# Optimization experiments

Hardware: AMD Instinct MI355X
Metric: run time of the kernel (lower is better)

The kernel has to match this reference:

```python
import jax, jax.numpy as jnp
import numpy as np

D_MODEL = 1024
NUM_HEADS = 16
DEPTH = D_MODEL // NUM_HEADS


def setup_inputs() -> dict:
    key = jax.random.key(0)
    ks = jax.random.split(key, 12)
    B, S = 4, 2048
    scale = 1.0 / np.sqrt(D_MODEL)
    inp = {
        "query": jax.random.normal(ks[0], (B, S, D_MODEL), jnp.float32),
        "key": jax.random.normal(ks[1], (B, S, D_MODEL), jnp.float32),
        "value": jax.random.normal(ks[2], (B, S, D_MODEL), jnp.float32),
        "mask": jnp.zeros((B, 1, 1, S), jnp.float32),  # 1.0 => masked position
        "wq": jax.random.normal(ks[3], (D_MODEL, D_MODEL), jnp.float32) * scale,
        "bq": jnp.zeros((D_MODEL,), jnp.float32),
        "wk": jax.random.normal(ks[4], (D_MODEL, D_MODEL), jnp.float32) * scale,
        "bk": jnp.zeros((D_MODEL,), jnp.float32),
        "wv": jax.random.normal(ks[5], (D_MODEL, D_MODEL), jnp.float32) * scale,
        "bv": jnp.zeros((D_MODEL,), jnp.float32),
        "wo": jax.random.normal(ks[6], (D_MODEL, D_MODEL), jnp.float32) * scale,
        "bo": jnp.zeros((D_MODEL,), jnp.float32),
    }
    return inp


def _split_heads(x, B):
    # (B, S, d_model) -> (B, H, S, depth)
    return x.reshape(B, -1, NUM_HEADS, DEPTH).transpose(0, 2, 1, 3)


def reference(query, key, value, mask, wq, bq, wk, bk, wv, bv, wo, bo):
    B, Sq, _ = query.shape
    q = _split_heads(query @ wq + bq, B)   # (B,H,Sq,dh)
    k = _split_heads(key @ wk + bk, B)     # (B,H,Sk,dh)
    v = _split_heads(value @ wv + bv, B)   # (B,H,Sk,dh)

    logits = jnp.einsum("bhqd,bhkd->bhqk", q, k) / jnp.sqrt(
        jnp.asarray(DEPTH, q.dtype))
    logits = logits + mask * (-1e9)
    attn = jax.nn.softmax(logits, axis=-1)
    ctx = jnp.einsum("bhqk,bhkd->bhqd", attn, v)
    ctx = ctx.transpose(0, 2, 1, 3).reshape(B, Sq, D_MODEL)
    return ctx @ wo + bo
```

## Files before the change

kernel.cpp:

```cpp
#include <hip/hip_runtime.h>
#include <stdint.h>


typedef unsigned short u16;
typedef __attribute__((ext_vector_type(8))) short bf16x8;
typedef __attribute__((ext_vector_type(4))) short bf16x4;
typedef __attribute__((ext_vector_type(4))) float f32x4;

#define LOG2E 1.4426950408889634f

__device__ __forceinline__ u16 f2bf(float f) {
  uint32_t u = __builtin_bit_cast(uint32_t, f);
  u += 0x7fffu + ((u >> 16) & 1u);
  return (u16)(u >> 16);
}
__device__ __forceinline__ uint32_t cvt_pk(float a, float b) {
  uint32_t r;
  asm("v_cvt_pk_bf16_f32 %0, %1, %2" : "=v"(r) : "v"(a), "v"(b));
  return r;
}
__device__ __forceinline__ void gload16(const u16* g, u16* l) {
  __builtin_amdgcn_global_load_lds(
      (const __attribute__((address_space(1))) uint32_t*)(const void*)g,
      (__attribute__((address_space(3))) uint32_t*)(void*)l, 16, 0, 0);
}
__device__ __forceinline__ f32x4 mfma16(bf16x4 a, bf16x4 b, f32x4 c) {
#if __has_builtin(__builtin_amdgcn_mfma_f32_16x16x16bf16_1k)
  return __builtin_amdgcn_mfma_f32_16x16x16bf16_1k(a, b, c, 0, 0, 0);
#else
  f32x4 d = c;
  asm volatile("v_mfma_f32_16x16x16_bf16 %0, %1, %2, %0"
               : "+v"(d) : "v"(a), "v"(b));
  return d;
#endif
}

__global__ __launch_bounds__(256) void convert_x(
    const float* __restrict__ X, u16* __restrict__ Xb)
{
  const size_t i = ((size_t)blockIdx.x * 256 + threadIdx.x) * 8;
  const float4 a = *(const float4*)(X + i);
  const float4 b = *(const float4*)(X + i + 4);
  uint4 o;
  o.x = cvt_pk(a.x, a.y); o.y = cvt_pk(a.z, a.w);
  o.z = cvt_pk(b.x, b.y); o.w = cvt_pk(b.z, b.w);
  *(uint4*)(Xb + i) = o;
}

__global__ __launch_bounds__(256) void prep_mask(
    const float* __restrict__ mask, float* __restrict__ M2)
{
  const int i = blockIdx.x * 256 + threadIdx.x;
  M2[i] = mask[i] * (-1.0e9f * LOG2E);
}

__global__ __launch_bounds__(256) void transpose_w(
    const float* __restrict__ W0, const float* __restrict__ W1,
    const float* __restrict__ W2, const float* __restrict__ W3,
    u16* __restrict__ Wt)
{
  const int z = blockIdx.z;
  const float* W = (z == 0) ? W0 : (z == 1) ? W1 : (z == 2) ? W2 : W3;
  u16* T = Wt + ((size_t)z << 20);
  const int n0 = blockIdx.x * 64, k0 = blockIdx.y * 64;
  const int tid = threadIdx.x;
  const int r = tid >> 4, c4 = (tid & 15) * 4;
  __shared__ float t[64][65];
#pragma unroll
  for (int j = 0; j < 4; ++j) {
    const int row = r + j * 16;
    const float4 v = *(const float4*)(W + (size_t)(k0 + row) * 1024 + n0 + c4);
    t[c4 + 0][row] = v.x; t[c4 + 1][row] = v.y;
    t[c4 + 2][row] = v.z; t[c4 + 3][row] = v.w;
  }
  __syncthreads();
#pragma unroll
  for (int j = 0; j < 4; ++j) {
    const int nrow = r + j * 16;
    uint2 o;
    o.x = cvt_pk(t[nrow][c4 + 0], t[nrow][c4 + 1]);
    o.y = cvt_pk(t[nrow][c4 + 2], t[nrow][c4 + 3]);
    *(uint2*)(T + (size_t)(n0 + nrow) * 1024 + k0 + c4) = o;
  }
}

__global__ __launch_bounds__(256) void gemm_proj(
    const u16* __restrict__ A, const u16* __restrict__ Wt,
    const float* __restrict__ Bi, u16* __restrict__ O16,
    float* __restrict__ O32, int mode)
{
  const int bid = blockIdx.x;
  const int nid = (bid & 7) * 64 + (bid >> 3);
  const int n0 = (nid & 7) * 128;
  const int m0 = (nid >> 3) * 128;
  const int tid = threadIdx.x;
  const int w = tid >> 6, l = tid & 63, lo = l & 15, hi = l >> 4;
  const int wr = w >> 1, wc = w & 1;

  __shared__ __align__(16) u16 As[2][4096];
  __shared__ __align__(16) u16 Bs[2][4096];

  const f32x4 fz = {0.f, 0.f, 0.f, 0.f};
  f32x4 acc[4][4];
#pragma unroll
  for (int m = 0; m < 4; ++m)
#pragma unroll
    for (int n = 0; n < 4; ++n) acc[m][n] = fz;

  const int srow = w * 32 + (l >> 2);
  const u16* ga = A  + (size_t)(m0 + srow) * 1024 + (l & 3) * 8;
  const u16* gb = Wt + (size_t)(n0 + srow) * 1024 + (l & 3) * 8;

#define GST(k0_, b_)                                        \
  do {                                                      \
    gload16(ga + (k0_),             &As[b_][w * 1024]);     \
    gload16(ga + (k0_) + 16 * 1024, &As[b_][w * 1024 + 512]); \
    gload16(gb + (k0_),             &Bs[b_][w * 1024]);     \
    gload16(gb + (k0_) + 16 * 1024, &Bs[b_][w * 1024 + 512]); \
  } while (0)

  GST(0, 0);
  __syncthreads();

  for (int kt = 0; kt < 32; ++kt) {
    const int cur = kt & 1;
    GST(((kt + 1) & 31) * 32, cur ^ 1);
    asm volatile("s_waitcnt vmcnt(4)" ::: "memory");
    __builtin_amdgcn_s_barrier();

    bf16x8 af[4], bf[4];
#pragma unroll
    for (int m = 0; m < 4; ++m)
      af[m] = *(const bf16x8*)&As[cur][(wr * 64 + m * 16 + lo) * 32 + hi * 8];
#pragma unroll
    for (int n = 0; n < 4; ++n)
      bf[n] = *(const bf16x8*)&Bs[cur][(wc * 64 + n * 16 + lo) * 32 + hi * 8];
#pragma unroll
    for (int m = 0; m < 4; ++m)
#pragma unroll
      for (int n = 0; n < 4; ++n)
        acc[m][n] = __builtin_amdgcn_mfma_f32_16x16x32_bf16(af[m], bf[n], acc[m][n], 0, 0, 0);

    asm volatile("s_waitcnt lgkmcnt(0)" ::: "memory");
    __builtin_amdgcn_s_barrier();
  }
#undef GST

#pragma unroll
  for (int m = 0; m < 4; ++m) {
#pragma unroll
    for (int n = 0; n < 4; ++n) {
      const int col = n0 + wc * 64 + n * 16 + lo;
      const float bc = Bi[col];
      const int h = col >> 6, d = col & 63;
#pragma unroll
      for (int i = 0; i < 4; ++i) {
        const int r = m0 + wr * 64 + m * 16 + hi * 4 + i;
        const int b = r >> 11, s = r & 2047;
        float v = acc[m][n][i] + bc;
        if (mode == 0) {
          v *= 0.125f * LOG2E;
          O16[((size_t)((b * 16 + h) * 2048 + s)) * 64 + d] = f2bf(v);
        } else if (mode == 1) {
          O16[((size_t)((b * 16 + h) * 2048 + s)) * 64 + d] = f2bf(v);
        } else if (mode == 2) {
          O16[((size_t)((b * 16 + h) * 64 + d)) * 2048 + s] = f2bf(v);
        } else {
          O32[(size_t)r * 1024 + col] = v;
        }
      }
    }
  }
}

__global__ __launch_bounds__(512, 4) void attn(
    const u16* __restrict__ Q, const u16* __restrict__ K,
    const u16* __restrict__ Vt, const float* __restrict__ M2,
    u16* __restrict__ Ctx)
{
  const int bid = blockIdx.x;
  const int nid = (bid & 7) * 64 + (bid >> 3);
  const int qt = nid & 7;
  const int bh = nid >> 3;
  const int b = bh >> 4, h = bh & 15;
  const int tid = threadIdx.x;
  const int w = tid >> 6, l = tid & 63, lo = l & 15, hi = l >> 4;

  __shared__ __align__(16) u16 Kl[2][4096];
  __shared__ __align__(16) u16 Vl[2][4096];
  __shared__ __align__(16) float Msk[2048];

  const u16* Qb = Q + (size_t)bh * (2048 * 64);
  const u16* Kb = K + (size_t)bh * (2048 * 64);
  const u16* Vb = Vt + (size_t)bh * (64 * 2048);

  *(float4*)&Msk[tid * 4] = *(const float4*)(M2 + (size_t)b * 2048 + tid * 4);

  const int qrow0 = qt * 256 + w * 32 + lo;
  const bf16x8 qa00 = *(const bf16x8*)(Qb + (size_t)qrow0 * 64 + hi * 8);
  const bf16x8 qa01 = *(const bf16x8*)(Qb + (size_t)qrow0 * 64 + 32 + hi * 8);
  const bf16x8 qa10 = *(const bf16x8*)(Qb + (size_t)(qrow0 + 16) * 64 + hi * 8);
  const bf16x8 qa11 = *(const bf16x8*)(Qb + (size_t)(qrow0 + 16) * 64 + 32 + hi * 8);

  const f32x4 fz = {0.f, 0.f, 0.f, 0.f};
  f32x4 o0[4] = {fz, fz, fz, fz};
  f32x4 o1[4] = {fz, fz, fz, fz};
  f32x4 ol0 = fz, ol1 = fz;
  const short oneb = (short)0x3F80;
  const bf16x4 ones = {oneb, oneb, oneb, oneb};
  const int lo7 = lo & 7;

  const int rowA = tid >> 3;
  const int slA  = (tid & 7) ^ (rowA & 7);
  const u16* gK = Kb + (size_t)rowA * 64 + slA * 8;
  const u16* gV = Vb + (size_t)rowA * 2048 + slA * 8;

#define STAGE(kt_, buf_)                                    \
  do {                                                      \
    gload16(gK + (size_t)(kt_) * 4096, &Kl[buf_][w * 512]); \
    gload16(gV + (kt_) * 64,           &Vl[buf_][w * 512]); \
  } while (0)

  STAGE(0, 0);
  __syncthreads();

  for (int kt = 0; kt < 32; ++kt) {
    const int cur = kt & 1;
    STAGE((kt + 1) & 31, cur ^ 1);
    asm volatile("s_waitcnt vmcnt(2)" ::: "memory");
    __builtin_amdgcn_s_barrier();

    const int kv0 = kt * 64;
    const u16* Kc = &Kl[cur][0];
    const u16* Vc = &Vl[cur][0];

    f32x4 st0[4], st1[4];
    __builtin_amdgcn_s_setprio(1);
#pragma unroll
    for (int f = 0; f < 4; ++f) {
      const int krow = (f * 16 + lo) * 64;
      const bf16x8 kb0 = *(const bf16x8*)&Kc[krow + ((hi ^ lo7) << 3)];
      const bf16x8 kb1 = *(const bf16x8*)&Kc[krow + (((4 + hi) ^ lo7) << 3)];
      const f32x4 c = *(const f32x4*)&Msk[kv0 + 16 * f + 4 * hi];
      f32x4 a0 = __builtin_amdgcn_mfma_f32_16x16x32_bf16(kb0, qa00, c, 0, 0, 0);
      st0[f] = __builtin_amdgcn_mfma_f32_16x16x32_bf16(kb1, qa01, a0, 0, 0, 0);
      f32x4 a1 = __builtin_amdgcn_mfma_f32_16x16x32_bf16(kb0, qa10, c, 0, 0, 0);
      st1[f] = __builtin_amdgcn_mfma_f32_16x16x32_bf16(kb1, qa11, a1, 0, 0, 0);
    }
    __builtin_amdgcn_s_setprio(0);

    union { uint32_t u[2]; bf16x4 v; } pa0[4], pa1[4];
#pragma unroll
    for (int f = 0; f < 4; ++f) {
      pa0[f].u[0] = cvt_pk(exp2f(st0[f][0]), exp2f(st0[f][1]));
      pa0[f].u[1] = cvt_pk(exp2f(st0[f][2]), exp2f(st0[f][3]));
      pa1[f].u[0] = cvt_pk(exp2f(st1[f][0]), exp2f(st1[f][1]));
      pa1[f].u[1] = cvt_pk(exp2f(st1[f][2]), exp2f(st1[f][3]));
    }

    __builtin_amdgcn_s_setprio(1);
#pragma unroll
    for (int f = 0; f < 4; ++f) {
      ol0 = mfma16(pa0[f].v, ones, ol0);
      ol1 = mfma16(pa1[f].v, ones, ol1);
#pragma unroll
      for (int nf = 0; nf < 4; ++nf) {
        const int vrow = (lo + 16 * nf) * 64;
        const int slot = (((2 * f + (hi >> 1)) ^ lo7) << 3) + ((hi & 1) << 2);
        const bf16x4 vb = *(const bf16x4*)&Vc[vrow + slot];
        o0[nf] = mfma16(pa0[f].v, vb, o0[nf]);
        o1[nf] = mfma16(pa1[f].v, vb, o1[nf]);
      }
    }
    __builtin_amdgcn_s_setprio(0);

    asm volatile("s_waitcnt lgkmcnt(0)" ::: "memory");
    __builtin_amdgcn_s_barrier();
  }
#undef STAGE

  float inv0[4], inv1[4];
#pragma unroll
  for (int i = 0; i < 4; ++i) { inv0[i] = 1.f / ol0[i]; inv1[i] = 1.f / ol1[i]; }
#pragma unroll
  for (int nf = 0; nf < 4; ++nf) {
#pragma unroll
    for (int i = 0; i < 4; ++i) {
      const int s0 = qt * 256 + w * 32 + hi * 4 + i;
      const int d = nf * 16 + lo;
      Ctx[((size_t)((b * 2048 + s0) * 16 + h)) * 64 + d] = f2bf(o0[nf][i] * inv0[i]);
      Ctx[((size_t)((b * 2048 + s0 + 16) * 16 + h)) * 64 + d] = f2bf(o1[nf][i] * inv1[i]);
    }
  }
}

extern "C" void kernel_launch(void* const* d_in, const int* in_sizes, int n_in,
                              void* d_out, int out_size, void* d_ws, size_t ws_size,
                              hipStream_t stream) {
  const float* q_in = (const float*)d_in[0];
  const float* k_in = (const float*)d_in[1];
  const float* v_in = (const float*)d_in[2];
  const float* mask = (const float*)d_in[3];
  const float* wq = (const float*)d_in[4];
  const float* bq = (const float*)d_in[5];
  const float* wk = (const float*)d_in[6];
  const float* bk = (const float*)d_in[7];
  const float* wv = (const float*)d_in[8];
  const float* bv = (const float*)d_in[9];
  const float* wo = (const float*)d_in[10];
  const float* bo = (const float*)d_in[11];

  u16* ws  = (u16*)d_ws;
  u16* wtq = ws;
  u16* wtk = wtq + (1u << 20);
  u16* wtv = wtk + (1u << 20);
  u16* wto = wtv + (1u << 20);
  u16* Qb  = wto + (1u << 20);
  u16* Kb  = Qb + (size_t)8192 * 1024;
  u16* Vtb = Kb + (size_t)8192 * 1024;
  u16* xbf = Vtb + (size_t)8192 * 1024;
  u16* ctx = xbf;
  float* M2 = (float*)(xbf + (size_t)8192 * 1024);

  transpose_w<<<dim3(16, 16, 4), 256, 0, stream>>>(wq, wk, wv, wo, wtq);
  prep_mask<<<32, 256, 0, stream>>>(mask, M2);

  convert_x<<<4096, 256, 0, stream>>>(q_in, xbf);
  gemm_proj<<<512, 256, 0, stream>>>(xbf, wtq, bq, Qb, nullptr, 0);
  convert_x<<<4096, 256, 0, stream>>>(k_in, xbf);
  gemm_proj<<<512, 256, 0, stream>>>(xbf, wtk, bk, Kb, nullptr, 1);
  convert_x<<<4096, 256, 0, stream>>>(v_in, xbf);
  gemm_proj<<<512, 256, 0, stream>>>(xbf, wtv, bv, Vtb, nullptr, 2);

  attn<<<512, 512, 0, stream>>>(Qb, Kb, Vtb, M2, ctx);

  gemm_proj<<<512, 256, 0, stream>>>(ctx, wto, bo, nullptr, (float*)d_out, 3);
}
```

Baseline: 264.9 us.

## Fuse fp32-to-bf16 input conversion into a single batched QKV projection GEMM

Drops the three convert_x kernels and loads fp32 activations directly in the projection GEMM, converting them to bf16 in registers before writing to padded LDS. The three Q/K/V projections run as one 1536-block launch instead of three 512-block launches. This removes the round trip of bf16 activation copies through global memory and several launches, and gives more blocks to fill the GPU. In exchange the A tile is staged through registers rather than async global-to-LDS loads, so the GEMM reads twice the bytes for A and adds conversion work inside the main loop.

```diff
diff --git a/kernel.cpp b/kernel.cpp
--- a/kernel.cpp
+++ b/kernel.cpp
@@ -33,18 +33,6 @@
                : "+v"(d) : "v"(a), "v"(b));
   return d;
 #endif
-}
-
-__global__ __launch_bounds__(256) void convert_x(
-    const float* __restrict__ X, u16* __restrict__ Xb)
-{
-  const size_t i = ((size_t)blockIdx.x * 256 + threadIdx.x) * 8;
-  const float4 a = *(const float4*)(X + i);
-  const float4 b = *(const float4*)(X + i + 4);
-  uint4 o;
-  o.x = cvt_pk(a.x, a.y); o.y = cvt_pk(a.z, a.w);
-  o.z = cvt_pk(b.x, b.y); o.w = cvt_pk(b.z, b.w);
-  *(uint4*)(Xb + i) = o;
 }
 
 __global__ __launch_bounds__(256) void prep_mask(
@@ -84,10 +72,132 @@
   }
 }
 
-__global__ __launch_bounds__(256) void gemm_proj(
+__global__ __launch_bounds__(256) void gemm_qkv(
+    const float* __restrict__ Xq, const float* __restrict__ Xk, const float* __restrict__ Xv,
+    const u16* __restrict__ Wt3,
+    const float* __restrict__ Bq, const float* __restrict__ Bk, const float* __restrict__ Bv,
+    u16* __restrict__ Qo, u16* __restrict__ Ko, u16* __restrict__ Vto)
+{
+  const int bid = blockIdx.x;
+  const int nid = (bid & 7) * 192 + (bid >> 3);
+  const int z = nid >> 9;
+  const int rem = nid & 511;
+  const int n0 = (rem & 7) * 128;
+  const int m0 = (rem >> 3) * 128;
+
+  const float* X = (z == 0) ? Xq : (z == 1) ? Xk : Xv;
+  const u16* Wt  = Wt3 + ((size_t)z << 20);
+  const float* Bi = (z == 0) ? Bq : (z == 1) ? Bk : Bv;
+
+  const int tid = threadIdx.x;
+  const int w = tid >> 6, l = tid & 63, lo = l & 15, hi = l >> 4;
+  const int wr = w >> 1, wc = w & 1;
+
+  __shared__ __align__(16) u16 As[2][128 * 40];
+  __shared__ __align__(16) u16 Bs[2][4096];
+
+  const f32x4 fz = {0.f, 0.f, 0.f, 0.f};
+  f32x4 acc[4][4];
+#pragma unroll
+  for (int m = 0; m < 4; ++m)
+#pragma unroll
+    for (int n = 0; n < 4; ++n) acc[m][n] = fz;
+
+  const int arow = tid >> 1, ahalf = (tid & 1) * 16;
+  const float* ga = X + (size_t)(m0 + arow) * 1024 + ahalf;
+  u16* awr0 = &As[0][arow * 40 + ahalf];
+  u16* awr1 = &As[1][arow * 40 + ahalf];
+  const int brow = w * 32 + (l >> 2);
+  const u16* gb = Wt + (size_t)(n0 + brow) * 1024 + (l & 3) * 8;
+
+  float4 ar0, ar1, ar2, ar3;
+#define A_LOAD(k0_)                         \
+  do {                                      \
+    const float* p_ = ga + (k0_);           \
+    ar0 = *(const float4*)(p_);             \
+    ar1 = *(const float4*)(p_ + 4);         \
+    ar2 = *(const float4*)(p_ + 8);         \
+    ar3 = *(const float4*)(p_ + 12);        \
+  } while (0)
+#define A_WRITE(dst_)                                      \
+  do {                                                     \
+    uint4 c0_, c1_;                                        \
+    c0_.x = cvt_pk(ar0.x, ar0.y); c0_.y = cvt_pk(ar0.z, ar0.w); \
+    c0_.z = cvt_pk(ar1.x, ar1.y); c0_.w = cvt_pk(ar1.z, ar1.w); \
+    c1_.x = cvt_pk(ar2.x, ar2.y); c1_.y = cvt_pk(ar2.z, ar2.w); \
+    c1_.z = cvt_pk(ar3.x, ar3.y); c1_.w = cvt_pk(ar3.z, ar3.w); \
+    *(uint4*)(dst_) = c0_;                                 \
+    *(uint4*)((dst_) + 8) = c1_;                           \
+  } while (0)
+#define B_STAGE(k0_, b_)                                    \
+  do {                                                      \
+    gload16(gb + (k0_),             &Bs[b_][w * 1024]);     \
+    gload16(gb + (k0_) + 16 * 1024, &Bs[b_][w * 1024 + 512]); \
+  } while (0)
+
+  A_LOAD(0);
+  B_STAGE(0, 0);
+  A_WRITE(awr0);
+  __syncthreads();
+
+  for (int kt = 0; kt < 32; ++kt) {
+    const int cur = kt & 1;
+    const int knx = ((kt + 1) & 31) * 32;
+    A_LOAD(knx);
+    B_STAGE(knx, cur ^ 1);
+    asm volatile("s_waitcnt vmcnt(6)" ::: "memory");
+    __builtin_amdgcn_s_barrier();
+
+    bf16x8 af[4], bf[4];
+#pragma unroll
+    for (int m = 0; m < 4; ++m)
+      af[m] = *(const bf16x8*)&As[cur][(wr * 64 + m * 16 + lo) * 40 + hi * 8];
+#pragma unroll
+    for (int n = 0; n < 4; ++n)
+      bf[n] = *(const bf16x8*)&Bs[cur][(wc * 64 + n * 16 + lo) * 32 + hi * 8];
+#pragma unroll
+    for (int m = 0; m < 4; ++m)
+#pragma unroll
+      for (int n = 0; n < 4; ++n)
+        acc[m][n] = __builtin_amdgcn_mfma_f32_16x16x32_bf16(af[m], bf[n], acc[m][n], 0, 0, 0);
+
+    A_WRITE(cur ? awr0 : awr1);
+
+    asm volatile("s_waitcnt lgkmcnt(0)" ::: "memory");
+    __builtin_amdgcn_s_barrier();
+  }
+#undef A_LOAD
+#undef A_WRITE
+#undef B_STAGE
+
+#pragma unroll
+  for (int m = 0; m < 4; ++m) {
+#pragma unroll
+    for (int n = 0; n < 4; ++n) {
+      const int col = n0 + wc * 64 + n * 16 + lo;
+      const float bc = Bi[col];
+      const int h = col >> 6, d = col & 63;
+#pragma unroll
+      for (int i = 0; i < 4; ++i) {
+        const int r = m0 + wr * 64 + m * 16 + hi * 4 + i;
+        const int b = r >> 11, s = r & 2047;
+        float v = acc[m][n][i] + bc;
+        if (z == 0) {
+          v *= 0.125f * LOG2E;
+          Qo[((size_t)((b * 16 + h) * 2048 + s)) * 64 + d] = f2bf(v);
+        } else if (z == 1) {
+          Ko[((size_t)((b * 16 + h) * 2048 + s)) * 64 + d] = f2bf(v);
+        } else {
+          Vto[((size_t)((b * 16 + h) * 64 + d)) * 2048 + s] = f2bf(v);
+        }
+      }
+    }
+  }
+}
+
+__global__ __launch_bounds__(256) void gemm_out(
     const u16* __restrict__ A, const u16* __restrict__ Wt,
-    const float* __restrict__ Bi, u16* __restrict__ O16,
-    float* __restrict__ O32, int mode)
+    const float* __restrict__ Bo, float* __restrict__ Out)
 {
   const int bid = blockIdx.x;
   const int nid = (bid & 7) * 64 + (bid >> 3);
@@ -151,23 +261,11 @@
 #pragma unroll
     for (int n = 0; n < 4; ++n) {
       const int col = n0 + wc * 64 + n * 16 + lo;
-      const float bc = Bi[col];
-      const int h = col >> 6, d = col & 63;
+      const float bc = Bo[col];
 #pragma unroll
       for (int i = 0; i < 4; ++i) {
         const int r = m0 + wr * 64 + m * 16 + hi * 4 + i;
-        const int b = r >> 11, s = r & 2047;
-        float v = acc[m][n][i] + bc;
-        if (mode == 0) {
-          v *= 0.125f * LOG2E;
-          O16[((size_t)((b * 16 + h) * 2048 + s)) * 64 + d] = f2bf(v);
-        } else if (mode == 1) {
-          O16[((size_t)((b * 16 + h) * 2048 + s)) * 64 + d] = f2bf(v);
-        } else if (mode == 2) {
-          O16[((size_t)((b * 16 + h) * 64 + d)) * 2048 + s] = f2bf(v);
-        } else {
-          O32[(size_t)r * 1024 + col] = v;
-        }
+        Out[(size_t)r * 1024 + col] = acc[m][n][i] + bc;
       }
     }
   }
@@ -312,27 +410,20 @@
 
   u16* ws  = (u16*)d_ws;
   u16* wtq = ws;
-  u16* wtk = wtq + (1u << 20);
-  u16* wtv = wtk + (1u << 20);
-  u16* wto = wtv + (1u << 20);
+  u16* wto = wtq + 3u * (1u << 20);
   u16* Qb  = wto + (1u << 20);
   u16* Kb  = Qb + (size_t)8192 * 1024;
   u16* Vtb = Kb + (size_t)8192 * 1024;
-  u16* xbf = Vtb + (size_t)8192 * 1024;
-  u16* ctx = xbf;
-  float* M2 = (float*)(xbf + (size_t)8192 * 1024);
+  u16* ctx = Vtb + (size_t)8192 * 1024;
+  float* M2 = (float*)(ctx + (size_t)8192 * 1024);
 
   transpose_w<<<dim3(16, 16, 4), 256, 0, stream>>>(wq, wk, wv, wo, wtq);
   prep_mask<<<32, 256, 0, stream>>>(mask, M2);
 
-  convert_x<<<4096, 256, 0, stream>>>(q_in, xbf);
-  gemm_proj<<<512, 256, 0, stream>>>(xbf, wtq, bq, Qb, nullptr, 0);
-  convert_x<<<4096, 256, 0, stream>>>(k_in, xbf);
-  gemm_proj<<<512, 256, 0, stream>>>(xbf, wtk, bk, Kb, nullptr, 1);
-  convert_x<<<4096, 256, 0, stream>>>(v_in, xbf);
-  gemm_proj<<<512, 256, 0, stream>>>(xbf, wtv, bv, Vtb, nullptr, 2);
+  gemm_qkv<<<1536, 256, 0, stream>>>(q_in, k_in, v_in, wtq,
+                                     bq, bk, bv, Qb, Kb, Vtb);
 
   attn<<<512, 512, 0, stream>>>(Qb, Kb, Vtb, M2, ctx);
 
-  gemm_proj<<<512, 256, 0, stream>>>(ctx, wto, bo, nullptr, (float*)d_out, 3);
-}
+  gemm_out<<<512, 256, 0, stream>>>(ctx, wto, bo, (float*)d_out);
+}
```

New measurement: 258.8 us. 2.3% less time.
